# Optimization experiments

Measured on AMD Instinct MI355X. Metric: run time of the kernel, lower is better.

Reference implementation:

```python
import jax, jax.numpy as jnp
import numpy as np

N_NODES = 100000
N_EDGES = 1600000
D_IN = 128
D_H = 128


def gcn_conv(x, src, dst, n, W, b):
    # PyG GCNConv: add self loops, symmetric normalization D^-1/2 (A+I) D^-1/2, then linear.
    h = x @ W  # [N, Dh]
    loop = jnp.arange(n)
    s = jnp.concatenate([src, loop])
    d = jnp.concatenate([dst, loop])
    deg = jax.ops.segment_sum(jnp.ones_like(d, dtype=h.dtype), d, num_segments=n)
    dinv = jnp.where(deg > 0, jax.lax.rsqrt(deg), 0.0)
    w = dinv[s] * dinv[d]  # [E+N]
    agg = jax.ops.segment_sum(h[s] * w[:, None], d, num_segments=n)
    return agg + b


def setup_inputs() -> dict:
    key = jax.random.key(0)
    ks = jax.random.split(key, 6)
    x = jax.random.normal(ks[0], (N_NODES, D_IN), dtype=jnp.float32)
    edge_index = jax.random.randint(ks[1], (2, N_EDGES), 0, N_NODES, dtype=jnp.int32)
    sc = 1.0 / np.sqrt(D_IN)
    W1 = jax.random.normal(ks[2], (D_IN, D_H), dtype=jnp.float32) * sc
    b1 = jnp.zeros((D_H,), jnp.float32)
    W2 = jax.random.normal(ks[3], (D_H, D_H), dtype=jnp.float32) * (1.0 / np.sqrt(D_H))
    b2 = jnp.zeros((D_H,), jnp.float32)
    Wm1 = jax.random.normal(ks[4], (2 * D_H, D_H), dtype=jnp.float32) * (1.0 / np.sqrt(2 * D_H))
    bm1 = jnp.zeros((D_H,), jnp.float32)
    Wm2 = jax.random.normal(ks[5], (D_H, 1), dtype=jnp.float32) * (1.0 / np.sqrt(D_H))
    bm2 = jnp.zeros((1,), jnp.float32)
    return {"x": x, "edge_index": edge_index, "W1": W1, "b1": b1, "W2": W2, "b2": b2,
            "Wm1": Wm1, "bm1": bm1, "Wm2": Wm2, "bm2": bm2}


def reference(x, edge_index, W1, b1, W2, b2, Wm1, bm1, Wm2, bm2):
    src, dst = edge_index[0], edge_index[1]
    n = x.shape[0]
    h = jax.nn.relu(gcn_conv(x, src, dst, n, W1, b1))  # dropout = identity at eval
    h = jax.nn.relu(gcn_conv(h, src, dst, n, W2, b2))
    ef = jnp.concatenate([h[src], h[dst]], axis=1)  # [E, 2*Dh]
    z = jax.nn.relu(ef @ Wm1 + bm1)
    logits = (z @ Wm2 + bm2).squeeze(-1)  # [E]
    return jax.nn.sigmoid(logits)
```

## Files before the change

kernel.cpp:

```cpp
#include <hip/hip_runtime.h>
#include <math.h>

#define NN 100000
#define NE 1600000
#define NB 391
#define PART 12500

typedef __attribute__((ext_vector_type(8))) short bf16x8;
typedef __attribute__((ext_vector_type(4))) float f32x4;

__device__ inline unsigned short f2bf(float f) {
  unsigned int u = __float_as_uint(f);
  u = u + 0x7fffu + ((u >> 16) & 1u);
  return (unsigned short)(u >> 16);
}
__device__ inline float bf2f(unsigned short h) {
  return __uint_as_float(((unsigned int)h) << 16);
}

__global__ __launch_bounds__(256) void k_zero(int* __restrict__ deg) {
  int i = blockIdx.x * 256 + threadIdx.x;
  if (i < NN) deg[i] = 0;
}

__global__ __launch_bounds__(256) void k_hist(const int* __restrict__ dst, int* __restrict__ deg) {
  int b = blockIdx.x;
  int xcd = b & 7;
  int e = (b >> 3) * 256 + threadIdx.x;
  int d = dst[e];
  if ((unsigned)(d - xcd * PART) < (unsigned)PART) atomicAdd(&deg[d], 1);
}

__global__ __launch_bounds__(256) void k_scan1(const int* __restrict__ deg, int* __restrict__ tmp,
                                               int* __restrict__ bsum) {
  __shared__ int wsum[4];
  int i = blockIdx.x * 256 + threadIdx.x;
  int v = (i < NN) ? deg[i] : 0;
  int x = v;
#pragma unroll
  for (int d = 1; d < 64; d <<= 1) {
    int y = __shfl_up(x, d);
    if ((threadIdx.x & 63) >= d) x += y;
  }
  if ((threadIdx.x & 63) == 63) wsum[threadIdx.x >> 6] = x;
  __syncthreads();
  int add = 0;
  for (int w = 0; w < (threadIdx.x >> 6); ++w) add += wsum[w];
  int incl = x + add;
  if (i < NN) tmp[i] = incl - v;
  if (threadIdx.x == 255) bsum[blockIdx.x] = incl;
}

__global__ void k_scan2(const int* __restrict__ bsum, int* __restrict__ boff) {
  int lane = threadIdx.x;
  int run = 0;
  for (int b0 = 0; b0 < NB; b0 += 64) {
    int i = b0 + lane;
    int v = (i < NB) ? bsum[i] : 0;
    int x = v;
#pragma unroll
    for (int d = 1; d < 64; d <<= 1) {
      int y = __shfl_up(x, d);
      if (lane >= d) x += y;
    }
    if (i < NB) boff[i] = run + x - v;
    run += __shfl(x, 63);
  }
}

__global__ __launch_bounds__(256) void k_scan3(const int* __restrict__ deg, int* __restrict__ tmp,
                                               const int* __restrict__ boff, int* __restrict__ rs,
                                               float* __restrict__ dinv) {
  int i = blockIdx.x * 256 + threadIdx.x;
  if (i < NN) {
    int v = tmp[i] + boff[blockIdx.x];
    rs[i] = v;
    tmp[i] = v;
    dinv[i] = rsqrtf((float)(deg[i] + 1));
  }
  if (i == 0) rs[NN] = NE;
}

__global__ __launch_bounds__(256) void k_fill(const int* __restrict__ src, const int* __restrict__ dst,
                                              int* __restrict__ cursor, uint2* __restrict__ sde) {
  int b = blockIdx.x;
  int xcd = b & 7;
  int e = (b >> 3) * 256 + threadIdx.x;
  int d = dst[e];
  int s = src[e];
  if ((unsigned)(d - xcd * PART) < (unsigned)PART) {
    int p = atomicAdd(&cursor[d], 1);
    unsigned int lo = (unsigned int)s | ((unsigned int)d << 17);
    unsigned int hi = ((unsigned int)d >> 15) | ((unsigned int)e << 2);
    sde[p] = make_uint2(lo, hi);
  }
}

__global__ __launch_bounds__(256) void k_prep(const float* __restrict__ W1, const float* __restrict__ W2,
                                              const float* __restrict__ Wm1, unsigned short* __restrict__ Bp) {
  int gid = blockIdx.x * 256 + threadIdx.x;
  int idx = gid & 16383;
  int m = gid >> 14;
  int u = idx & 7;
  int lane = (idx >> 3) & 63;
  int ft = idx >> 9;
  int t = ft & 3, f = ft >> 2;
  int n = f * 16 + (lane & 15);
  int k = t * 32 + (lane >> 4) * 8 + u;
  const float* Wsrc = (m == 0) ? W1 : (m == 1) ? W2 : Wm1;
  int krow = (m == 3) ? (k + 128) : k;
  Bp[gid] = f2bf(Wsrc[(size_t)krow * 128 + n]);
}

__global__ __launch_bounds__(256) void k_gemm_mfma(const unsigned short* __restrict__ A,
                                                   const unsigned short* __restrict__ Bp,
                                                   unsigned short* __restrict__ Y,
                                                   const float* __restrict__ scale, int nrows) {
  __shared__ unsigned short BL[16384];
  {
    const uint4* gp = (const uint4*)Bp;
    uint4* sp = (uint4*)BL;
#pragma unroll
    for (int i = 0; i < 8; ++i) sp[threadIdx.x + i * 256] = gp[threadIdx.x + i * 256];
  }
  __syncthreads();

  const int w = threadIdx.x >> 6, lane = threadIdx.x & 63;
  const int r = lane & 15, g = lane >> 4;
  const int rowbase = blockIdx.x * 64 + w * 16;
  const int arow = rowbase + r;

  bf16x8 av[4];
  if (arow < nrows) {
#pragma unroll
    for (int t = 0; t < 4; ++t) av[t] = *(const bf16x8*)(A + (size_t)arow * 128 + g * 8 + t * 32);
  } else {
#pragma unroll
    for (int t = 0; t < 4; ++t) av[t] = (bf16x8){0, 0, 0, 0, 0, 0, 0, 0};
  }

  f32x4 acc[8];
#pragma unroll
  for (int f = 0; f < 8; ++f) acc[f] = (f32x4){0.f, 0.f, 0.f, 0.f};

#pragma unroll
  for (int f = 0; f < 8; ++f)
#pragma unroll
    for (int t = 0; t < 4; ++t) {
      bf16x8 bv = *(const bf16x8*)(&BL[(((f << 2) | t) << 9) | (lane << 3)]);
      acc[f] = __builtin_amdgcn_mfma_f32_16x16x32_bf16(av[t], bv, acc[f], 0, 0, 0);
    }

#pragma unroll
  for (int j = 0; j < 4; ++j) {
    int row = rowbase + g * 4 + j;
    if (row < nrows) {
      float sc = scale ? scale[row] : 1.f;
#pragma unroll
      for (int f = 0; f < 8; ++f) Y[(size_t)row * 128 + f * 16 + r] = f2bf(acc[f][j] * sc);
    }
  }
}

__global__ __launch_bounds__(256) void k_gemm_mfma_f32(const float* __restrict__ A,
                                                       const unsigned short* __restrict__ Bp,
                                                       unsigned short* __restrict__ Y,
                                                       const float* __restrict__ scale, int nrows) {
  __shared__ unsigned short BL[16384];
  {
    const uint4* gp = (const uint4*)Bp;
    uint4* sp = (uint4*)BL;
#pragma unroll
    for (int i = 0; i < 8; ++i) sp[threadIdx.x + i * 256] = gp[threadIdx.x + i * 256];
  }
  __syncthreads();

  const int w = threadIdx.x >> 6, lane = threadIdx.x & 63;
  const int r = lane & 15, g = lane >> 4;
  const int rowbase = blockIdx.x * 64 + w * 16;
  const int arow = rowbase + r;

  bf16x8 av[4];
  if (arow < nrows) {
#pragma unroll
    for (int t = 0; t < 4; ++t) {
      float4 a0 = *(const float4*)(A + (size_t)arow * 128 + g * 8 + t * 32);
      float4 a1 = *(const float4*)(A + (size_t)arow * 128 + g * 8 + t * 32 + 4);
      bf16x8 pk;
      pk[0] = (short)f2bf(a0.x); pk[1] = (short)f2bf(a0.y);
      pk[2] = (short)f2bf(a0.z); pk[3] = (short)f2bf(a0.w);
      pk[4] = (short)f2bf(a1.x); pk[5] = (short)f2bf(a1.y);
      pk[6] = (short)f2bf(a1.z); pk[7] = (short)f2bf(a1.w);
      av[t] = pk;
    }
  } else {
#pragma unroll
    for (int t = 0; t < 4; ++t) av[t] = (bf16x8){0, 0, 0, 0, 0, 0, 0, 0};
  }

  f32x4 acc[8];
#pragma unroll
  for (int f = 0; f < 8; ++f) acc[f] = (f32x4){0.f, 0.f, 0.f, 0.f};

#pragma unroll
  for (int f = 0; f < 8; ++f)
#pragma unroll
    for (int t = 0; t < 4; ++t) {
      bf16x8 bv = *(const bf16x8*)(&BL[(((f << 2) | t) << 9) | (lane << 3)]);
      acc[f] = __builtin_amdgcn_mfma_f32_16x16x32_bf16(av[t], bv, acc[f], 0, 0, 0);
    }

#pragma unroll
  for (int j = 0; j < 4; ++j) {
    int row = rowbase + g * 4 + j;
    if (row < nrows) {
      float sc = scale ? scale[row] : 1.f;
#pragma unroll
      for (int f = 0; f < 8; ++f) Y[(size_t)row * 128 + f * 16 + r] = f2bf(acc[f][j] * sc);
    }
  }
}

__global__ __launch_bounds__(512) void k_gemm_dual(const unsigned short* __restrict__ A,
                                                   const unsigned short* __restrict__ Bp2,
                                                   unsigned short* __restrict__ U,
                                                   unsigned short* __restrict__ V, int nrows) {
  __shared__ unsigned short BL[32768];
  {
    const uint4* gp = (const uint4*)Bp2;
    uint4* sp = (uint4*)BL;
#pragma unroll
    for (int i = 0; i < 8; ++i) sp[threadIdx.x + i * 512] = gp[threadIdx.x + i * 512];
  }
  __syncthreads();

  const int w = threadIdx.x >> 6, lane = threadIdx.x & 63;
  const int r = lane & 15, g = lane >> 4;
  const int rowbase = blockIdx.x * 128 + w * 16;
  const int arow = rowbase + r;

  bf16x8 av[4];
  if (arow < nrows) {
#pragma unroll
    for (int t = 0; t < 4; ++t) av[t] = *(const bf16x8*)(A + (size_t)arow * 128 + g * 8 + t * 32);
  } else {
#pragma unroll
    for (int t = 0; t < 4; ++t) av[t] = (bf16x8){0, 0, 0, 0, 0, 0, 0, 0};
  }

  f32x4 accU[8], accV[8];
#pragma unroll
  for (int f = 0; f < 8; ++f) {
    accU[f] = (f32x4){0.f, 0.f, 0.f, 0.f};
    accV[f] = (f32x4){0.f, 0.f, 0.f, 0.f};
  }

#pragma unroll
  for (int f = 0; f < 8; ++f)
#pragma unroll
    for (int t = 0; t < 4; ++t) {
      bf16x8 bu = *(const bf16x8*)(&BL[(((f << 2) | t) << 9) | (lane << 3)]);
      bf16x8 bv = *(const bf16x8*)(&BL[16384 + ((((f << 2) | t) << 9) | (lane << 3))]);
      accU[f] = __builtin_amdgcn_mfma_f32_16x16x32_bf16(av[t], bu, accU[f], 0, 0, 0);
      accV[f] = __builtin_amdgcn_mfma_f32_16x16x32_bf16(av[t], bv, accV[f], 0, 0, 0);
    }

#pragma unroll
  for (int j = 0; j < 4; ++j) {
    int row = rowbase + g * 4 + j;
    if (row < nrows) {
#pragma unroll
      for (int f = 0; f < 8; ++f) {
        U[(size_t)row * 128 + f * 16 + r] = f2bf(accU[f][j]);
        V[(size_t)row * 128 + f * 16 + r] = f2bf(accV[f][j]);
      }
    }
  }
}

__global__ __launch_bounds__(256) void k_agg(const unsigned short* __restrict__ T,
                                             const int* __restrict__ rs, const uint2* __restrict__ sde,
                                             const float* __restrict__ dinv, const float* __restrict__ bias,
                                             unsigned short* __restrict__ outB) {
  int node = blockIdx.x * 4 + (threadIdx.x >> 6);
  if (node >= NN) return;
  int lane = threadIdx.x & 63;
  int beg = rs[node], end = rs[node + 1];
  float dn = dinv[node];

  unsigned int sv = *(const unsigned int*)(T + (size_t)node * 128 + lane * 2);
  float ax = bf2f((unsigned short)(sv & 0xffff));
  float ay = bf2f((unsigned short)(sv >> 16));
  float bx = 0.f, by = 0.f;

  for (int j0 = beg; j0 < end; j0 += 64) {
    int sl = (j0 + lane < end) ? (int)(sde[j0 + lane].x & 0x1FFFFu) : 0;
    int n = end - j0;
    if (n > 64) n = 64;
    int c = 0;
    for (; c + 2 <= n; c += 2) {
      int s0 = __builtin_amdgcn_readlane(sl, c);
      int s1 = __builtin_amdgcn_readlane(sl, c + 1);
      unsigned int h0 = *(const unsigned int*)(T + (size_t)s0 * 128 + lane * 2);
      unsigned int h1 = *(const unsigned int*)(T + (size_t)s1 * 128 + lane * 2);
      ax += bf2f((unsigned short)(h0 & 0xffff));
      ay += bf2f((unsigned short)(h0 >> 16));
      bx += bf2f((unsigned short)(h1 & 0xffff));
      by += bf2f((unsigned short)(h1 >> 16));
    }
    if (c < n) {
      int s0 = __builtin_amdgcn_readlane(sl, c);
      unsigned int h0 = *(const unsigned int*)(T + (size_t)s0 * 128 + lane * 2);
      ax += bf2f((unsigned short)(h0 & 0xffff));
      ay += bf2f((unsigned short)(h0 >> 16));
    }
  }
  ax += bx;
  ay += by;

  float2 bb = *(const float2*)(bias + lane * 2);
  float ox = fmaxf(fmaf(dn, ax, bb.x), 0.f);
  float oy = fmaxf(fmaf(dn, ay, bb.y), 0.f);
  unsigned int pv = (unsigned int)f2bf(ox) | ((unsigned int)f2bf(oy) << 16);
  *(unsigned int*)(outB + (size_t)node * 128 + lane * 2) = pv;
}

__global__ __launch_bounds__(256) void k_edge(const unsigned short* __restrict__ u,
                                              const unsigned short* __restrict__ v,
                                              const uint2* __restrict__ sde,
                                              const float* __restrict__ bm1, const float* __restrict__ Wm2,
                                              const float* __restrict__ bm2, float* __restrict__ out) {
  __shared__ float red[4][32 * 65];
  const int w = threadIdx.x >> 6;
  const int lane = threadIdx.x & 63;
  float* __restrict__ myred = &red[w][0];

  const int bat = blockIdx.x * 4 + w;
  const int jb = bat * 64;

  float2 bmv = *(const float2*)(bm1 + lane * 2);
  float2 w2 = *(const float2*)(Wm2 + lane * 2);
  const float b2 = bm2[0];

  const uint2 ev = sde[jb + lane];

  int cur = -1;
  float vb0 = 0.f, vb1 = 0.f;

#pragma unroll
  for (int h2 = 0; h2 < 2; ++h2) {
#pragma unroll 8
    for (int c = 0; c < 32; ++c) {
      int idx = h2 * 32 + c;
      unsigned int lo = (unsigned int)__builtin_amdgcn_readlane((int)ev.x, idx);
      unsigned int hi = (unsigned int)__builtin_amdgcn_readlane((int)ev.y, idx);
      int s = (int)(lo & 0x1FFFFu);
      int d = (int)((lo >> 17) | ((hi & 3u) << 15));
      unsigned int uu = *(const unsigned int*)(u + (size_t)s * 128 + lane * 2);
      if (d != cur) {
        unsigned int vv = *(const unsigned int*)(v + (size_t)d * 128 + lane * 2);
        vb0 = bf2f((unsigned short)(vv & 0xffff)) + bmv.x;
        vb1 = bf2f((unsigned short)(vv >> 16)) + bmv.y;
        cur = d;
      }
      float z0 = fmaxf(bf2f((unsigned short)(uu & 0xffff)) + vb0, 0.f);
      float z1 = fmaxf(bf2f((unsigned short)(uu >> 16)) + vb1, 0.f);
      myred[c * 65 + lane] = fmaf(z0, w2.x, z1 * w2.y);
    }
    __syncthreads();

    int cr = lane & 31, hh = lane >> 5;
    const float* row = &myred[cr * 65 + hh * 32];
    float s0 = 0.f, s1 = 0.f;
#pragma unroll
    for (int k = 0; k < 32; k += 2) {
      s0 += row[k];
      s1 += row[k + 1];
    }
    float s = s0 + s1;
    s += __shfl_xor(s, 32);
    float sg = 1.f / (1.f + __expf(-(s + b2)));
    unsigned int hi2 = (unsigned int)__shfl((int)ev.y, h2 * 32 + cr);
    int eid = (int)(hi2 >> 2);
    if (hh == 0) out[eid] = sg;
    __syncthreads();
  }
}

extern "C" void kernel_launch(void* const* d_in, const int* in_sizes, int n_in,
                              void* d_out, int out_size, void* d_ws, size_t ws_size,
                              hipStream_t stream) {
  const float* x   = (const float*)d_in[0];
  const int* ei    = (const int*)d_in[1];
  const float* W1  = (const float*)d_in[2];
  const float* b1  = (const float*)d_in[3];
  const float* W2  = (const float*)d_in[4];
  const float* b2  = (const float*)d_in[5];
  const float* Wm1 = (const float*)d_in[6];
  const float* bm1 = (const float*)d_in[7];
  const float* Wm2 = (const float*)d_in[8];
  const float* bm2 = (const float*)d_in[9];
  float* out = (float*)d_out;

  const int* src = ei;
  const int* dst = ei + NE;

  char* ws = (char*)d_ws;
  int*   deg    = (int*)(ws + 0x000000);
  int*   rs     = (int*)(ws + 0x080000);
  int*   cursor = (int*)(ws + 0x100000);
  float* dinv   = (float*)(ws + 0x180000);
  int*   bsum   = (int*)(ws + 0x200000);
  int*   boff   = (int*)(ws + 0x210000);
  unsigned short* Bp = (unsigned short*)(ws + 0x220000);
  uint2* sde    = (uint2*)(ws + 0x240000);
  unsigned short* bufT = (unsigned short*)(ws + 0xE80000);
  unsigned short* hbuf = (unsigned short*)(ws + 0x2700000);
  unsigned short* vbuf = (unsigned short*)(ws + 0x4000000);
  unsigned short* ubuf = bufT;

  const int gN = NB;
  const int gPart = (NE / 256) * 8;
  const int gRow = (NN + 63) / 64;
  const int gDual = (NN + 127) / 128;
  const int gAgg = (NN + 3) / 4;
  const int gEdge = 25000 / 4;

  k_zero<<<gN, 256, 0, stream>>>(deg);
  k_hist<<<gPart, 256, 0, stream>>>(dst, deg);
  k_scan1<<<gN, 256, 0, stream>>>(deg, cursor, bsum);
  k_scan2<<<1, 64, 0, stream>>>(bsum, boff);
  k_scan3<<<gN, 256, 0, stream>>>(deg, cursor, boff, rs, dinv);
  k_fill<<<gPart, 256, 0, stream>>>(src, dst, cursor, sde);
  k_prep<<<256, 256, 0, stream>>>(W1, W2, Wm1, Bp);

  k_gemm_mfma_f32<<<gRow, 256, 0, stream>>>(x, Bp, bufT, dinv, NN);
  k_agg<<<gAgg, 256, 0, stream>>>(bufT, rs, sde, dinv, b1, hbuf);

  k_gemm_mfma<<<gRow, 256, 0, stream>>>(hbuf, Bp + 16384, bufT, dinv, NN);
  k_agg<<<gAgg, 256, 0, stream>>>(bufT, rs, sde, dinv, b2, hbuf);

  k_gemm_dual<<<gDual, 512, 0, stream>>>(hbuf, Bp + 2 * 16384, ubuf, vbuf, NN);

  k_edge<<<gEdge, 256, 0, stream>>>(ubuf, vbuf, sde, bm1, Wm2, bm2, out);
}
```

Measured before the change: 457.1 us.

## Use 16-byte row gathers with four rows per wavefront in aggregation and edge kernels

```diff
diff --git a/kernel.cpp b/kernel.cpp
--- a/kernel.cpp
+++ b/kernel.cpp
@@ -16,6 +16,10 @@
 }
 __device__ inline float bf2f(unsigned short h) {
   return __uint_as_float(((unsigned int)h) << 16);
+}
+__device__ inline void unpk(unsigned int w, float& a, float& b) {
+  a = __uint_as_float(w << 16);
+  b = __uint_as_float(w & 0xffff0000u);
 }
 
 __global__ __launch_bounds__(256) void k_zero(int* __restrict__ deg) {
@@ -285,44 +289,61 @@
   int node = blockIdx.x * 4 + (threadIdx.x >> 6);
   if (node >= NN) return;
   int lane = threadIdx.x & 63;
+  int q = lane >> 4, r = lane & 15;
   int beg = rs[node], end = rs[node + 1];
   float dn = dinv[node];
 
-  unsigned int sv = *(const unsigned int*)(T + (size_t)node * 128 + lane * 2);
-  float ax = bf2f((unsigned short)(sv & 0xffff));
-  float ay = bf2f((unsigned short)(sv >> 16));
-  float bx = 0.f, by = 0.f;
+  float acc[8];
+#pragma unroll
+  for (int i = 0; i < 8; ++i) acc[i] = 0.f;
 
   for (int j0 = beg; j0 < end; j0 += 64) {
     int sl = (j0 + lane < end) ? (int)(sde[j0 + lane].x & 0x1FFFFu) : 0;
     int n = end - j0;
     if (n > 64) n = 64;
-    int c = 0;
-    for (; c + 2 <= n; c += 2) {
-      int s0 = __builtin_amdgcn_readlane(sl, c);
-      int s1 = __builtin_amdgcn_readlane(sl, c + 1);
-      unsigned int h0 = *(const unsigned int*)(T + (size_t)s0 * 128 + lane * 2);
-      unsigned int h1 = *(const unsigned int*)(T + (size_t)s1 * 128 + lane * 2);
-      ax += bf2f((unsigned short)(h0 & 0xffff));
-      ay += bf2f((unsigned short)(h0 >> 16));
-      bx += bf2f((unsigned short)(h1 & 0xffff));
-      by += bf2f((unsigned short)(h1 >> 16));
-    }
-    if (c < n) {
-      int s0 = __builtin_amdgcn_readlane(sl, c);
-      unsigned int h0 = *(const unsigned int*)(T + (size_t)s0 * 128 + lane * 2);
-      ax += bf2f((unsigned short)(h0 & 0xffff));
-      ay += bf2f((unsigned short)(h0 >> 16));
-    }
-  }
-  ax += bx;
-  ay += by;
-
-  float2 bb = *(const float2*)(bias + lane * 2);
-  float ox = fmaxf(fmaf(dn, ax, bb.x), 0.f);
-  float oy = fmaxf(fmaf(dn, ay, bb.y), 0.f);
-  unsigned int pv = (unsigned int)f2bf(ox) | ((unsigned int)f2bf(oy) << 16);
-  *(unsigned int*)(outB + (size_t)node * 128 + lane * 2) = pv;
+#pragma unroll 4
+    for (int c = 0; c * 4 < n; ++c) {
+      int idx = (c << 2) | q;
+      int s = __shfl(sl, idx);
+      if (idx < n) {
+        uint4 hv = *(const uint4*)(T + (size_t)s * 128 + r * 8);
+        float f0, f1, f2, f3, f4, f5, f6, f7;
+        unpk(hv.x, f0, f1); unpk(hv.y, f2, f3);
+        unpk(hv.z, f4, f5); unpk(hv.w, f6, f7);
+        acc[0] += f0; acc[1] += f1; acc[2] += f2; acc[3] += f3;
+        acc[4] += f4; acc[5] += f5; acc[6] += f6; acc[7] += f7;
+      }
+    }
+  }
+
+#pragma unroll
+  for (int i = 0; i < 8; ++i) {
+    acc[i] += __shfl_xor(acc[i], 16);
+    acc[i] += __shfl_xor(acc[i], 32);
+  }
+
+  uint4 sv = *(const uint4*)(T + (size_t)node * 128 + r * 8);
+  float s0, s1, s2, s3, s4, s5, s6, s7;
+  unpk(sv.x, s0, s1); unpk(sv.y, s2, s3);
+  unpk(sv.z, s4, s5); unpk(sv.w, s6, s7);
+  float4 ba = *(const float4*)(bias + r * 8);
+  float4 bb = *(const float4*)(bias + r * 8 + 4);
+  float o0 = fmaxf(fmaf(dn, acc[0] + s0, ba.x), 0.f);
+  float o1 = fmaxf(fmaf(dn, acc[1] + s1, ba.y), 0.f);
+  float o2 = fmaxf(fmaf(dn, acc[2] + s2, ba.z), 0.f);
+  float o3 = fmaxf(fmaf(dn, acc[3] + s3, ba.w), 0.f);
+  float o4 = fmaxf(fmaf(dn, acc[4] + s4, bb.x), 0.f);
+  float o5 = fmaxf(fmaf(dn, acc[5] + s5, bb.y), 0.f);
+  float o6 = fmaxf(fmaf(dn, acc[6] + s6, bb.z), 0.f);
+  float o7 = fmaxf(fmaf(dn, acc[7] + s7, bb.w), 0.f);
+  if (q == 0) {
+    uint4 pv;
+    pv.x = (unsigned int)f2bf(o0) | ((unsigned int)f2bf(o1) << 16);
+    pv.y = (unsigned int)f2bf(o2) | ((unsigned int)f2bf(o3) << 16);
+    pv.z = (unsigned int)f2bf(o4) | ((unsigned int)f2bf(o5) << 16);
+    pv.w = (unsigned int)f2bf(o6) | ((unsigned int)f2bf(o7) << 16);
+    *(uint4*)(outB + (size_t)node * 128 + r * 8) = pv;
+  }
 }
 
 __global__ __launch_bounds__(256) void k_edge(const unsigned short* __restrict__ u,
@@ -330,60 +351,80 @@
                                               const uint2* __restrict__ sde,
                                               const float* __restrict__ bm1, const float* __restrict__ Wm2,
                                               const float* __restrict__ bm2, float* __restrict__ out) {
-  __shared__ float red[4][32 * 65];
+  __shared__ float red[4][16 * 65];
   const int w = threadIdx.x >> 6;
   const int lane = threadIdx.x & 63;
+  const int q = lane >> 4, r = lane & 15;
   float* __restrict__ myred = &red[w][0];
 
-  const int bat = blockIdx.x * 4 + w;
-  const int jb = bat * 64;
-
-  float2 bmv = *(const float2*)(bm1 + lane * 2);
-  float2 w2 = *(const float2*)(Wm2 + lane * 2);
+  const int jb = (blockIdx.x * 4 + w) * 64;
+
+  float bmv[8], w2[8];
+  {
+    float4 a = *(const float4*)(bm1 + r * 8);
+    float4 b = *(const float4*)(bm1 + r * 8 + 4);
+    bmv[0] = a.x; bmv[1] = a.y; bmv[2] = a.z; bmv[3] = a.w;
+    bmv[4] = b.x; bmv[5] = b.y; bmv[6] = b.z; bmv[7] = b.w;
+    float4 c = *(const float4*)(Wm2 + r * 8);
+    float4 d = *(const float4*)(Wm2 + r * 8 + 4);
+    w2[0] = c.x; w2[1] = c.y; w2[2] = c.z; w2[3] = c.w;
+    w2[4] = d.x; w2[5] = d.y; w2[6] = d.z; w2[7] = d.w;
+  }
   const float b2 = bm2[0];
 
   const uint2 ev = sde[jb + lane];
+  const int sl = (int)(ev.x & 0x1FFFFu);
+  const int dl = (int)((ev.x >> 17) | ((ev.y & 3u) << 15));
 
   int cur = -1;
-  float vb0 = 0.f, vb1 = 0.f;
-
-#pragma unroll
-  for (int h2 = 0; h2 < 2; ++h2) {
-#pragma unroll 8
-    for (int c = 0; c < 32; ++c) {
-      int idx = h2 * 32 + c;
-      unsigned int lo = (unsigned int)__builtin_amdgcn_readlane((int)ev.x, idx);
-      unsigned int hi = (unsigned int)__builtin_amdgcn_readlane((int)ev.y, idx);
-      int s = (int)(lo & 0x1FFFFu);
-      int d = (int)((lo >> 17) | ((hi & 3u) << 15));
-      unsigned int uu = *(const unsigned int*)(u + (size_t)s * 128 + lane * 2);
-      if (d != cur) {
-        unsigned int vv = *(const unsigned int*)(v + (size_t)d * 128 + lane * 2);
-        vb0 = bf2f((unsigned short)(vv & 0xffff)) + bmv.x;
-        vb1 = bf2f((unsigned short)(vv >> 16)) + bmv.y;
-        cur = d;
-      }
-      float z0 = fmaxf(bf2f((unsigned short)(uu & 0xffff)) + vb0, 0.f);
-      float z1 = fmaxf(bf2f((unsigned short)(uu >> 16)) + vb1, 0.f);
-      myred[c * 65 + lane] = fmaf(z0, w2.x, z1 * w2.y);
-    }
-    __syncthreads();
-
-    int cr = lane & 31, hh = lane >> 5;
-    const float* row = &myred[cr * 65 + hh * 32];
+  float vb[8];
+#pragma unroll
+  for (int i = 0; i < 8; ++i) vb[i] = 0.f;
+
+#pragma unroll 4
+  for (int c = 0; c < 16; ++c) {
+    int idx = (c << 2) | q;
+    int s = __shfl(sl, idx);
+    int d = __shfl(dl, idx);
+    uint4 uu = *(const uint4*)(u + (size_t)s * 128 + r * 8);
+    if (d != cur) {
+      uint4 vv = *(const uint4*)(v + (size_t)d * 128 + r * 8);
+      float g0, g1, g2, g3, g4, g5, g6, g7;
+      unpk(vv.x, g0, g1); unpk(vv.y, g2, g3);
+      unpk(vv.z, g4, g5); unpk(vv.w, g6, g7);
+      vb[0] = g0 + bmv[0]; vb[1] = g1 + bmv[1];
+      vb[2] = g2 + bmv[2]; vb[3] = g3 + bmv[3];
+      vb[4] = g4 + bmv[4]; vb[5] = g5 + bmv[5];
+      vb[6] = g6 + bmv[6]; vb[7] = g7 + bmv[7];
+      cur = d;
+    }
+    float f0, f1, f2, f3, f4, f5, f6, f7;
+    unpk(uu.x, f0, f1); unpk(uu.y, f2, f3);
+    unpk(uu.z, f4, f5); unpk(uu.w, f6, f7);
+    float p = 0.f;
+    p = fmaf(fmaxf(f0 + vb[0], 0.f), w2[0], p);
+    p = fmaf(fmaxf(f1 + vb[1], 0.f), w2[1], p);
+    p = fmaf(fmaxf(f2 + vb[2], 0.f), w2[2], p);
+    p = fmaf(fmaxf(f3 + vb[3], 0.f), w2[3], p);
+    p = fmaf(fmaxf(f4 + vb[4], 0.f), w2[4], p);
+    p = fmaf(fmaxf(f5 + vb[5], 0.f), w2[5], p);
+    p = fmaf(fmaxf(f6 + vb[6], 0.f), w2[6], p);
+    p = fmaf(fmaxf(f7 + vb[7], 0.f), w2[7], p);
+    myred[c * 65 + q * 16 + r] = p;
+  }
+  __syncthreads();
+
+  {
+    const float* row = &myred[(lane >> 2) * 65 + (lane & 3) * 16];
     float s0 = 0.f, s1 = 0.f;
 #pragma unroll
-    for (int k = 0; k < 32; k += 2) {
+    for (int k = 0; k < 16; k += 2) {
       s0 += row[k];
       s1 += row[k + 1];
     }
-    float s = s0 + s1;
-    s += __shfl_xor(s, 32);
-    float sg = 1.f / (1.f + __expf(-(s + b2)));
-    unsigned int hi2 = (unsigned int)__shfl((int)ev.y, h2 * 32 + cr);
-    int eid = (int)(hi2 >> 2);
-    if (hh == 0) out[eid] = sg;
-    __syncthreads();
+    float logit = s0 + s1 + b2;
+    int eid = (int)(ev.y >> 2);
+    out[eid] = 1.f / (1.f + __expf(-logit));
   }
 }
 
```

Measured after the change: 409.8 us. 1.12x faster.
